# Kernel tuning notes

Hardware: AMD Instinct MI355X
Metric: run time of the kernel (lower is better)

Reference implementation:

```python
import jax, jax.numpy as jnp
import numpy as np

B, N, ATTR, H, OUT, STEPS = 8, 4096, 16, 64, 1, 8


def setup_inputs() -> dict:
    key = jax.random.key(0)
    ks = jax.random.split(key, 12)
    attr_matrix = jax.random.normal(ks[0], (B, N, ATTR), jnp.float32)
    adj_matrix = (jax.random.uniform(ks[1], (B, N, N)) < 0.01).astype(jnp.float32)
    s = float(1.0 / np.sqrt(H))
    u = lambda k, shape: jax.random.uniform(k, shape, jnp.float32, -s, s)
    Wi = jax.random.normal(ks[2], (H, ATTR), jnp.float32) * float(np.sqrt(2.0 / ATTR))  # kaiming
    bi = jnp.zeros((H,), jnp.float32)
    Wz = u(ks[3], (H, 3 * H)); bz = u(ks[4], (H,))
    Wr = u(ks[5], (H, 3 * H)); br = u(ks[6], (H,))
    Wh = u(ks[7], (H, 3 * H)); bh = u(ks[8], (H,))
    Wo = jax.random.normal(ks[9], (OUT, H), jnp.float32) * float(np.sqrt(2.0 / (H + OUT)))  # xavier
    bo = jnp.zeros((OUT,), jnp.float32)
    return dict(attr_matrix=attr_matrix, adj_matrix=adj_matrix, Wi=Wi, bi=bi,
                Wz=Wz, bz=bz, Wr=Wr, br=br, Wh=Wh, bh=bh, Wo=Wo, bo=bo)


def reference(attr_matrix, adj_matrix, Wi, bi, Wz, bz, Wr, br, Wh, bh, Wo, bo):
    # initial node states: (B, N, H)
    h = jax.nn.relu(attr_matrix @ Wi.T + bi)
    A_in = adj_matrix
    A_out = jnp.swapaxes(adj_matrix, -1, -2)
    for _ in range(STEPS):
        a_in = jnp.einsum('bij,bjh->bih', A_in, h)
        a_out = jnp.einsum('bij,bjh->bih', A_out, h)
        inp = jnp.concatenate([a_in, a_out], axis=-1)           # (B, N, 2H)
        xs = jnp.concatenate([inp, h], axis=-1)                  # (B, N, 3H)
        z = jax.nn.sigmoid(xs @ Wz.T + bz)
        r = jax.nn.sigmoid(xs @ Wr.T + br)
        hn = jnp.tanh(jnp.concatenate([inp, r * h], axis=-1) @ Wh.T + bh)
        h = (1.0 - z) * h + z * hn
    return h @ Wo.T + bo  # (B, N, OUT)
```

## Files before the change

kernel.cpp:

```cpp
#include <hip/hip_runtime.h>
#include <hip/hip_fp16.h>
#include <stdint.h>

#define BB 8
#define NN 4096
#define ATTRD 16
#define HD 64
#define STEPS 8
#define NODES (BB*NN)
#define ECAP 96
#define KPAD 196

typedef _Float16 half8 __attribute__((ext_vector_type(8)));
typedef float floatx4 __attribute__((ext_vector_type(4)));
typedef unsigned long long ull;

__global__ void init_h_kernel(const float* __restrict__ attr, const float* __restrict__ Wi,
                              const float* __restrict__ bi, float* __restrict__ h,
                              __half* __restrict__ h16) {
    int idx = blockIdx.x * blockDim.x + threadIdx.x;
    if (idx >= (NODES + 1) * HD) return;
    if (idx >= NODES * HD) {
        h16[idx] = __float2half(0.f);
        return;
    }
    int node = idx >> 6, l = idx & 63;
    const float* a = attr + node * ATTRD;
    const float* w = Wi + l * ATTRD;
    float acc = bi[l];
#pragma unroll
    for (int k = 0; k < ATTRD; k++) acc += a[k] * w[k];
    float r = acc > 0.f ? acc : 0.f;
    h[idx] = r;
    h16[idx] = __float2half(r);
}

__global__ void wprep_kernel(const float* __restrict__ Wz, const float* __restrict__ Wr,
                             const float* __restrict__ Wh,
                             _Float16* __restrict__ wf_hi, _Float16* __restrict__ wf_lo) {
    int t = blockIdx.x * blockDim.x + threadIdx.x;
    if (t >= 3 * 4 * 6 * 64 * 8) return;
    int mat = t / 12288, rem = t % 12288;
    int tile = rem / 3072, rem2 = rem % 3072;
    int kc = rem2 / 512, rem3 = rem2 % 512;
    int lane = rem3 / 8, j = rem3 % 8;
    int k = kc * 32 + (lane >> 4) * 8 + j;
    int och = tile * 16 + (lane & 15);
    const float* W = (mat == 0) ? Wz : (mat == 1) ? Wr : Wh;
    float v = W[och * 192 + k];
    _Float16 hi = (_Float16)v;
    wf_hi[t] = hi;
    wf_lo[t] = (_Float16)(v - (float)hi);
}

__global__ __launch_bounds__(256) void count_rows_kernel(const float4* __restrict__ A4,
                                                         int* __restrict__ cnt_in,
                                                         int* __restrict__ edge_in,
                                                         int* __restrict__ cnt_out,
                                                         int* __restrict__ edge_out) {
    int wave = threadIdx.x >> 6, l = threadIdx.x & 63;
    int row = blockIdx.x * 4 + wave;
    const float4* rp = A4 + (size_t)row * 1024;
    ull mask_lt = (l == 63) ? ~0ull >> 1 : ((1ull << (l + 1)) - 1) >> 1;
    float4 v[16];
#pragma unroll
    for (int t = 0; t < 16; t++) v[t] = rp[t * 64 + l];
    int colbase = (row >> 12) << 12;
    int run = 0;
    int* erow = edge_in + row * ECAP;
#pragma unroll
    for (int t = 0; t < 16; t++) {
        ull b0 = __ballot(v[t].x != 0.f);
        ull b1 = __ballot(v[t].y != 0.f);
        ull b2 = __ballot(v[t].z != 0.f);
        ull b3 = __ballot(v[t].w != 0.f);
        int pre = __popcll(b0 & mask_lt) + __popcll(b1 & mask_lt) +
                  __popcll(b2 & mask_lt) + __popcll(b3 & mask_lt);
        float vv[4] = {v[t].x, v[t].y, v[t].z, v[t].w};
        int jbase = (t * 64 + l) * 4;
        int inner = 0;
#pragma unroll
        for (int q = 0; q < 4; q++) {
            if (vv[q] != 0.f) {
                int col = colbase | (jbase + q);
                int slot = run + pre + inner;
                if (slot < ECAP) erow[slot] = col;
                inner++;
                int s2 = atomicAdd(&cnt_out[col], 1);
                if (s2 < ECAP) edge_out[col * ECAP + s2] = row;
            }
        }
        run += __popcll(b0) + __popcll(b1) + __popcll(b2) + __popcll(b3);
    }
    if (l == 0) cnt_in[row] = run;
}

__global__ __launch_bounds__(256) void aggregate_kernel(
        const uint4* __restrict__ h4, const float* __restrict__ h,
        const int* __restrict__ cnt_in, const int* __restrict__ edge_in,
        const int* __restrict__ cnt_out, const int* __restrict__ edge_out,
        float* __restrict__ xs) {
    int bid = blockIdx.x;
    int batch = bid & 7;
    int group = bid >> 3;
    int wave = threadIdx.x >> 6;
    int node = (batch << 12) + group * 4 + wave;
    int l = threadIdx.x & 63;
    int sub = l >> 3;
    int part = l & 7;
    int ni = cnt_in[node];  if (ni > ECAP) ni = ECAP;
    int no = cnt_out[node]; if (no > ECAP) no = ECAP;
    const int* ei = edge_in + node * ECAP;
    const int* eo = edge_out + node * ECAP;
    int ei0 = ei[l], ei1 = ei[64 + (l & 31)];
    int eo0 = eo[l], eo1 = eo[64 + (l & 31)];
    float ai0 = 0.f, ai1 = 0.f, ai2 = 0.f, ai3 = 0.f, ai4 = 0.f, ai5 = 0.f, ai6 = 0.f, ai7 = 0.f;
    float ao0 = 0.f, ao1 = 0.f, ao2 = 0.f, ao3 = 0.f, ao4 = 0.f, ao5 = 0.f, ao6 = 0.f, ao7 = 0.f;
    int nmax = ni > no ? ni : no;
    for (int s = 0; s < nmax; s += 8) {
        int il = s + sub;
        int gi = (il < 64) ? __shfl(ei0, il) : __shfl(ei1, il - 64);
        int go = (il < 64) ? __shfl(eo0, il) : __shfl(eo1, il - 64);
        gi = (il < ni) ? gi : NODES;
        go = (il < no) ? go : NODES;
        uint4 gA = h4[(gi << 3) | part];
        uint4 gB = h4[(go << 3) | part];
        float2 pA0 = __half22float2(*(__half2*)&gA.x);
        float2 pA1 = __half22float2(*(__half2*)&gA.y);
        float2 pA2 = __half22float2(*(__half2*)&gA.z);
        float2 pA3 = __half22float2(*(__half2*)&gA.w);
        ai0 += pA0.x; ai1 += pA0.y; ai2 += pA1.x; ai3 += pA1.y;
        ai4 += pA2.x; ai5 += pA2.y; ai6 += pA3.x; ai7 += pA3.y;
        float2 pB0 = __half22float2(*(__half2*)&gB.x);
        float2 pB1 = __half22float2(*(__half2*)&gB.y);
        float2 pB2 = __half22float2(*(__half2*)&gB.z);
        float2 pB3 = __half22float2(*(__half2*)&gB.w);
        ao0 += pB0.x; ao1 += pB0.y; ao2 += pB1.x; ao3 += pB1.y;
        ao4 += pB2.x; ao5 += pB2.y; ao6 += pB3.x; ao7 += pB3.y;
    }
#pragma unroll
    for (int off = 8; off < 64; off <<= 1) {
        ai0 += __shfl_xor(ai0, off); ai1 += __shfl_xor(ai1, off);
        ai2 += __shfl_xor(ai2, off); ai3 += __shfl_xor(ai3, off);
        ai4 += __shfl_xor(ai4, off); ai5 += __shfl_xor(ai5, off);
        ai6 += __shfl_xor(ai6, off); ai7 += __shfl_xor(ai7, off);
        ao0 += __shfl_xor(ao0, off); ao1 += __shfl_xor(ao1, off);
        ao2 += __shfl_xor(ao2, off); ao3 += __shfl_xor(ao3, off);
        ao4 += __shfl_xor(ao4, off); ao5 += __shfl_xor(ao5, off);
        ao6 += __shfl_xor(ao6, off); ao7 += __shfl_xor(ao7, off);
    }
    if (l < 8) {
        float* dst = xs + node * 192;
        float4 si0 = {ai0, ai1, ai2, ai3};
        float4 si1 = {ai4, ai5, ai6, ai7};
        float4 so0 = {ao0, ao1, ao2, ao3};
        float4 so1 = {ao4, ao5, ao6, ao7};
        *(float4*)(dst + l * 8)          = si0;
        *(float4*)(dst + l * 8 + 4)      = si1;
        *(float4*)(dst + 64 + l * 8)     = so0;
        *(float4*)(dst + 64 + l * 8 + 4) = so1;
    }
    xs[node * 192 + 128 + l] = h[(node << 6) | l];
}

__global__ __launch_bounds__(256) void gate_kernel(
        const float* __restrict__ xs_g,
        const _Float16* __restrict__ wf_hi, const _Float16* __restrict__ wf_lo,
        const float* __restrict__ bz, const float* __restrict__ br,
        const float* __restrict__ bh,
        float* __restrict__ h, __half* __restrict__ h16) {
    __shared__ float xs_t[16][KPAD];
    int bid = blockIdx.x;
    int base = ((bid & 7) << 12) | ((bid >> 3) << 4);
    int tid = threadIdx.x;
    {
        const float4* src = (const float4*)(xs_g + base * 192);
#pragma unroll
        for (int i = 0; i < 3; i++) {
            int idx = tid + i * 256;
            float4 v = src[idx];
            int nl = idx / 48, kb = (idx % 48) * 4;
            *(float4*)&xs_t[nl][kb] = v;
        }
    }
    __syncthreads();
    int wave = tid >> 6, lane = tid & 63;
    int m = lane & 15, q = lane >> 4;
    int ch = wave * 16 + m;
    const half8* WH = (const half8*)wf_hi;
    const half8* WL = (const half8*)wf_lo;

    floatx4 accz = {0.f, 0.f, 0.f, 0.f};
    floatx4 accr = {0.f, 0.f, 0.f, 0.f};
#pragma unroll
    for (int kc = 0; kc < 6; kc++) {
        const float* xr = &xs_t[m][kc * 32 + q * 8];
        float4 xa = *(const float4*)xr;
        float4 xb = *(const float4*)(xr + 4);
        float xv[8] = {xa.x, xa.y, xa.z, xa.w, xb.x, xb.y, xb.z, xb.w};
        half8 ahi, alo;
#pragma unroll
        for (int j = 0; j < 8; j++) {
            _Float16 hj = (_Float16)xv[j];
            ahi[j] = hj;
            alo[j] = (_Float16)(xv[j] - (float)hj);
        }
        half8 bzh = WH[((0 * 4 + wave) * 6 + kc) * 64 + lane];
        half8 bzl = WL[((0 * 4 + wave) * 6 + kc) * 64 + lane];
        half8 brh = WH[((1 * 4 + wave) * 6 + kc) * 64 + lane];
        half8 brl = WL[((1 * 4 + wave) * 6 + kc) * 64 + lane];
        accz = __builtin_amdgcn_mfma_f32_16x16x32_f16(ahi, bzh, accz, 0, 0, 0);
        accz = __builtin_amdgcn_mfma_f32_16x16x32_f16(alo, bzh, accz, 0, 0, 0);
        accz = __builtin_amdgcn_mfma_f32_16x16x32_f16(ahi, bzl, accz, 0, 0, 0);
        accr = __builtin_amdgcn_mfma_f32_16x16x32_f16(ahi, brh, accr, 0, 0, 0);
        accr = __builtin_amdgcn_mfma_f32_16x16x32_f16(alo, brh, accr, 0, 0, 0);
        accr = __builtin_amdgcn_mfma_f32_16x16x32_f16(ahi, brl, accr, 0, 0, 0);
    }
    float bzv = bz[ch], brv = br[ch], bhv = bh[ch];
    float zreg[4], hvreg[4], rh[4];
#pragma unroll
    for (int rg = 0; rg < 4; rg++) {
        int nl = q * 4 + rg;
        float z = 1.f / (1.f + __expf(-(accz[rg] + bzv)));
        float r = 1.f / (1.f + __expf(-(accr[rg] + brv)));
        float hv = xs_t[nl][128 + ch];
        zreg[rg] = z; hvreg[rg] = hv; rh[rg] = r * hv;
    }
    __syncthreads();
#pragma unroll
    for (int rg = 0; rg < 4; rg++) xs_t[q * 4 + rg][128 + ch] = rh[rg];
    __syncthreads();

    floatx4 acch = {0.f, 0.f, 0.f, 0.f};
#pragma unroll
    for (int kc = 0; kc < 6; kc++) {
        const float* xr = &xs_t[m][kc * 32 + q * 8];
        float4 xa = *(const float4*)xr;
        float4 xb = *(const float4*)(xr + 4);
        float xv[8] = {xa.x, xa.y, xa.z, xa.w, xb.x, xb.y, xb.z, xb.w};
        half8 ahi, alo;
#pragma unroll
        for (int j = 0; j < 8; j++) {
            _Float16 hj = (_Float16)xv[j];
            ahi[j] = hj;
            alo[j] = (_Float16)(xv[j] - (float)hj);
        }
        half8 bhh = WH[((2 * 4 + wave) * 6 + kc) * 64 + lane];
        half8 bhl = WL[((2 * 4 + wave) * 6 + kc) * 64 + lane];
        acch = __builtin_amdgcn_mfma_f32_16x16x32_f16(ahi, bhh, acch, 0, 0, 0);
        acch = __builtin_amdgcn_mfma_f32_16x16x32_f16(alo, bhh, acch, 0, 0, 0);
        acch = __builtin_amdgcn_mfma_f32_16x16x32_f16(ahi, bhl, acch, 0, 0, 0);
    }
    __syncthreads();
#pragma unroll
    for (int rg = 0; rg < 4; rg++) {
        int nl = q * 4 + rg;
        float pre = acch[rg] + bhv;
        float th = 2.f / (1.f + __expf(-2.f * pre)) - 1.f;
        float hv = hvreg[rg];
        xs_t[nl][ch] = hv + zreg[rg] * (th - hv);
    }
    __syncthreads();
    {
        int f = tid * 4;
        int nl = f >> 6, c = f & 63;
        float4 v = *(const float4*)&xs_t[nl][c];
        int gi = ((base + nl) << 6) | c;
        *(float4*)&h[gi] = v;
        __half2 p0 = {__float2half(v.x), __float2half(v.y)};
        __half2 p1 = {__float2half(v.z), __float2half(v.w)};
        *(__half2*)&h16[gi] = p0;
        *(__half2*)&h16[gi + 2] = p1;
    }
}

__global__ void out_kernel(const float* __restrict__ h, const float* __restrict__ Wo,
                           const float* __restrict__ bo, float* __restrict__ out) {
    int wid = (blockIdx.x * blockDim.x + threadIdx.x) >> 6;
    int l = threadIdx.x & 63;
    if (wid >= NODES) return;
    float p = h[(wid << 6) | l] * Wo[l];
#pragma unroll
    for (int off = 32; off > 0; off >>= 1) p += __shfl_down(p, off);
    if (l == 0) out[wid] = p + bo[0];
}

extern "C" void kernel_launch(void* const* d_in, const int* in_sizes, int n_in,
                              void* d_out, int out_size, void* d_ws, size_t ws_size,
                              hipStream_t stream) {
    const float* attr = (const float*)d_in[0];
    const float* adj  = (const float*)d_in[1];
    const float* Wi   = (const float*)d_in[2];
    const float* bi   = (const float*)d_in[3];
    const float* Wz   = (const float*)d_in[4];
    const float* bz   = (const float*)d_in[5];
    const float* Wr   = (const float*)d_in[6];
    const float* br   = (const float*)d_in[7];
    const float* Wh   = (const float*)d_in[8];
    const float* bh   = (const float*)d_in[9];
    const float* Wo   = (const float*)d_in[10];
    const float* bo   = (const float*)d_in[11];
    float* out = (float*)d_out;

    char* ws = (char*)d_ws;
    size_t off = 0;
    auto carve = [&](size_t bytes) { void* p = ws + off; off = (off + bytes + 255) & ~(size_t)255; return p; };
    float* h      = (float*)carve((size_t)NODES * HD * 4);
    __half* h16   = (__half*)carve((size_t)(NODES + 1) * HD * 2);
    float* xs     = (float*)carve((size_t)NODES * 192 * 4);
    _Float16* wf_hi = (_Float16*)carve(3 * 4 * 6 * 64 * 8 * 2);
    _Float16* wf_lo = (_Float16*)carve(3 * 4 * 6 * 64 * 8 * 2);
    int* cnt_in   = (int*)carve((size_t)NODES * 4);
    int* cnt_out  = (int*)carve((size_t)NODES * 4);
    int* edge_in  = (int*)carve((size_t)NODES * ECAP * 4);
    int* edge_out = (int*)carve((size_t)NODES * ECAP * 4);

    hipMemsetAsync(cnt_out, 0, (size_t)NODES * 4, stream);

    init_h_kernel<<<((NODES + 1) * HD + 255) / 256, 256, 0, stream>>>(attr, Wi, bi, h, h16);
    wprep_kernel<<<(3 * 4 * 6 * 64 * 8 + 255) / 256, 256, 0, stream>>>(Wz, Wr, Wh, wf_hi, wf_lo);
    count_rows_kernel<<<NODES / 4, 256, 0, stream>>>((const float4*)adj, cnt_in, edge_in,
                                                     cnt_out, edge_out);

    for (int step = 0; step < STEPS; ++step) {
        aggregate_kernel<<<NODES / 4, 256, 0, stream>>>(
            (const uint4*)h16, h, cnt_in, edge_in, cnt_out, edge_out, xs);
        gate_kernel<<<NODES / 16, 256, 0, stream>>>(xs, wf_hi, wf_lo, bz, br, bh, h, h16);
    }
    out_kernel<<<NODES * HD / 256, 256, 0, stream>>>(h, Wo, bo, out);
}
```

Before: 1.182 ms.

## Fuse neighbor aggregation into the GRU gate kernel with ping-pong half buffers

Merges the separate aggregate and gate kernels into a single per-step kernel. Each wave now gathers neighbor sums for four nodes straight into the shared-memory xs tile, so the 192-wide fp32 xs array no longer makes a round trip through global memory and one launch per step is removed. The fp16 hidden-state copy is double-buffered between steps, because other blocks still read neighbor states while this block writes its new ones. The gather loop also handles 16 neighbors per iteration, giving more loads in flight. In exchange there are four times fewer blocks in the gather phase and each wave processes its nodes one after another, which may reduce latency hiding for the irregular loads.

```diff
diff --git a/kernel.cpp b/kernel.cpp
--- a/kernel.cpp
+++ b/kernel.cpp
@@ -17,11 +17,12 @@
 
 __global__ void init_h_kernel(const float* __restrict__ attr, const float* __restrict__ Wi,
                               const float* __restrict__ bi, float* __restrict__ h,
-                              __half* __restrict__ h16) {
+                              __half* __restrict__ h16a, __half* __restrict__ h16b) {
     int idx = blockIdx.x * blockDim.x + threadIdx.x;
     if (idx >= (NODES + 1) * HD) return;
     if (idx >= NODES * HD) {
-        h16[idx] = __float2half(0.f);
+        h16a[idx] = __float2half(0.f);
+        h16b[idx] = __float2half(0.f);
         return;
     }
     int node = idx >> 6, l = idx & 63;
@@ -32,7 +33,7 @@
     for (int k = 0; k < ATTRD; k++) acc += a[k] * w[k];
     float r = acc > 0.f ? acc : 0.f;
     h[idx] = r;
-    h16[idx] = __float2half(r);
+    h16a[idx] = __float2half(r);
 }
 
 __global__ void wprep_kernel(const float* __restrict__ Wz, const float* __restrict__ Wr,
@@ -95,96 +96,103 @@
     if (l == 0) cnt_in[row] = run;
 }
 
-__global__ __launch_bounds__(256) void aggregate_kernel(
-        const uint4* __restrict__ h4, const float* __restrict__ h,
+__global__ __launch_bounds__(256) void step_kernel(
+        const uint4* __restrict__ h4,
         const int* __restrict__ cnt_in, const int* __restrict__ edge_in,
         const int* __restrict__ cnt_out, const int* __restrict__ edge_out,
-        float* __restrict__ xs) {
-    int bid = blockIdx.x;
-    int batch = bid & 7;
-    int group = bid >> 3;
-    int wave = threadIdx.x >> 6;
-    int node = (batch << 12) + group * 4 + wave;
-    int l = threadIdx.x & 63;
-    int sub = l >> 3;
-    int part = l & 7;
-    int ni = cnt_in[node];  if (ni > ECAP) ni = ECAP;
-    int no = cnt_out[node]; if (no > ECAP) no = ECAP;
-    const int* ei = edge_in + node * ECAP;
-    const int* eo = edge_out + node * ECAP;
-    int ei0 = ei[l], ei1 = ei[64 + (l & 31)];
-    int eo0 = eo[l], eo1 = eo[64 + (l & 31)];
-    float ai0 = 0.f, ai1 = 0.f, ai2 = 0.f, ai3 = 0.f, ai4 = 0.f, ai5 = 0.f, ai6 = 0.f, ai7 = 0.f;
-    float ao0 = 0.f, ao1 = 0.f, ao2 = 0.f, ao3 = 0.f, ao4 = 0.f, ao5 = 0.f, ao6 = 0.f, ao7 = 0.f;
-    int nmax = ni > no ? ni : no;
-    for (int s = 0; s < nmax; s += 8) {
-        int il = s + sub;
-        int gi = (il < 64) ? __shfl(ei0, il) : __shfl(ei1, il - 64);
-        int go = (il < 64) ? __shfl(eo0, il) : __shfl(eo1, il - 64);
-        gi = (il < ni) ? gi : NODES;
-        go = (il < no) ? go : NODES;
-        uint4 gA = h4[(gi << 3) | part];
-        uint4 gB = h4[(go << 3) | part];
-        float2 pA0 = __half22float2(*(__half2*)&gA.x);
-        float2 pA1 = __half22float2(*(__half2*)&gA.y);
-        float2 pA2 = __half22float2(*(__half2*)&gA.z);
-        float2 pA3 = __half22float2(*(__half2*)&gA.w);
-        ai0 += pA0.x; ai1 += pA0.y; ai2 += pA1.x; ai3 += pA1.y;
-        ai4 += pA2.x; ai5 += pA2.y; ai6 += pA3.x; ai7 += pA3.y;
-        float2 pB0 = __half22float2(*(__half2*)&gB.x);
-        float2 pB1 = __half22float2(*(__half2*)&gB.y);
-        float2 pB2 = __half22float2(*(__half2*)&gB.z);
-        float2 pB3 = __half22float2(*(__half2*)&gB.w);
-        ao0 += pB0.x; ao1 += pB0.y; ao2 += pB1.x; ao3 += pB1.y;
-        ao4 += pB2.x; ao5 += pB2.y; ao6 += pB3.x; ao7 += pB3.y;
-    }
-#pragma unroll
-    for (int off = 8; off < 64; off <<= 1) {
-        ai0 += __shfl_xor(ai0, off); ai1 += __shfl_xor(ai1, off);
-        ai2 += __shfl_xor(ai2, off); ai3 += __shfl_xor(ai3, off);
-        ai4 += __shfl_xor(ai4, off); ai5 += __shfl_xor(ai5, off);
-        ai6 += __shfl_xor(ai6, off); ai7 += __shfl_xor(ai7, off);
-        ao0 += __shfl_xor(ao0, off); ao1 += __shfl_xor(ao1, off);
-        ao2 += __shfl_xor(ao2, off); ao3 += __shfl_xor(ao3, off);
-        ao4 += __shfl_xor(ao4, off); ao5 += __shfl_xor(ao5, off);
-        ao6 += __shfl_xor(ao6, off); ao7 += __shfl_xor(ao7, off);
-    }
-    if (l < 8) {
-        float* dst = xs + node * 192;
-        float4 si0 = {ai0, ai1, ai2, ai3};
-        float4 si1 = {ai4, ai5, ai6, ai7};
-        float4 so0 = {ao0, ao1, ao2, ao3};
-        float4 so1 = {ao4, ao5, ao6, ao7};
-        *(float4*)(dst + l * 8)          = si0;
-        *(float4*)(dst + l * 8 + 4)      = si1;
-        *(float4*)(dst + 64 + l * 8)     = so0;
-        *(float4*)(dst + 64 + l * 8 + 4) = so1;
-    }
-    xs[node * 192 + 128 + l] = h[(node << 6) | l];
-}
-
-__global__ __launch_bounds__(256) void gate_kernel(
-        const float* __restrict__ xs_g,
         const _Float16* __restrict__ wf_hi, const _Float16* __restrict__ wf_lo,
         const float* __restrict__ bz, const float* __restrict__ br,
         const float* __restrict__ bh,
-        float* __restrict__ h, __half* __restrict__ h16) {
+        float* __restrict__ h,
+        __half* __restrict__ h16o) {
     __shared__ float xs_t[16][KPAD];
     int bid = blockIdx.x;
     int base = ((bid & 7) << 12) | ((bid >> 3) << 4);
     int tid = threadIdx.x;
+    int wave = tid >> 6, l = tid & 63;
+
     {
-        const float4* src = (const float4*)(xs_g + base * 192);
-#pragma unroll
-        for (int i = 0; i < 3; i++) {
-            int idx = tid + i * 256;
-            float4 v = src[idx];
-            int nl = idx / 48, kb = (idx % 48) * 4;
-            *(float4*)&xs_t[nl][kb] = v;
+        int sub = l >> 3;
+        int part = l & 7;
+        for (int nn = 0; nn < 4; nn++) {
+            int row = wave * 4 + nn;
+            int node = base + row;
+            int ni = cnt_in[node];  if (ni > ECAP) ni = ECAP;
+            int no = cnt_out[node]; if (no > ECAP) no = ECAP;
+            const int* ei = edge_in + node * ECAP;
+            const int* eo = edge_out + node * ECAP;
+            int ei0 = ei[l], ei1 = ei[64 + (l & 31)];
+            int eo0 = eo[l], eo1 = eo[64 + (l & 31)];
+            float hslot = h[(node << 6) | l];
+            float ai0 = 0.f, ai1 = 0.f, ai2 = 0.f, ai3 = 0.f, ai4 = 0.f, ai5 = 0.f, ai6 = 0.f, ai7 = 0.f;
+            float ao0 = 0.f, ao1 = 0.f, ao2 = 0.f, ao3 = 0.f, ao4 = 0.f, ao5 = 0.f, ao6 = 0.f, ao7 = 0.f;
+            int nmax = ni > no ? ni : no;
+            for (int s = 0; s < nmax; s += 16) {
+                int ila = s + sub, ilb = s + 8 + sub;
+                int gia = (ila < 64) ? __shfl(ei0, ila) : __shfl(ei1, ila - 64);
+                int gib = (ilb < 64) ? __shfl(ei0, ilb) : __shfl(ei1, ilb - 64);
+                int goa = (ila < 64) ? __shfl(eo0, ila) : __shfl(eo1, ila - 64);
+                int gob = (ilb < 64) ? __shfl(eo0, ilb) : __shfl(eo1, ilb - 64);
+                gia = (ila < ni) ? gia : NODES;
+                gib = (ilb < ni) ? gib : NODES;
+                goa = (ila < no) ? goa : NODES;
+                gob = (ilb < no) ? gob : NODES;
+                uint4 gA = h4[(gia << 3) | part];
+                uint4 gB = h4[(gib << 3) | part];
+                uint4 gC = h4[(goa << 3) | part];
+                uint4 gD = h4[(gob << 3) | part];
+                float2 pA0 = __half22float2(*(__half2*)&gA.x);
+                float2 pA1 = __half22float2(*(__half2*)&gA.y);
+                float2 pA2 = __half22float2(*(__half2*)&gA.z);
+                float2 pA3 = __half22float2(*(__half2*)&gA.w);
+                ai0 += pA0.x; ai1 += pA0.y; ai2 += pA1.x; ai3 += pA1.y;
+                ai4 += pA2.x; ai5 += pA2.y; ai6 += pA3.x; ai7 += pA3.y;
+                float2 pB0 = __half22float2(*(__half2*)&gB.x);
+                float2 pB1 = __half22float2(*(__half2*)&gB.y);
+                float2 pB2 = __half22float2(*(__half2*)&gB.z);
+                float2 pB3 = __half22float2(*(__half2*)&gB.w);
+                ai0 += pB0.x; ai1 += pB0.y; ai2 += pB1.x; ai3 += pB1.y;
+                ai4 += pB2.x; ai5 += pB2.y; ai6 += pB3.x; ai7 += pB3.y;
+                float2 pC0 = __half22float2(*(__half2*)&gC.x);
+                float2 pC1 = __half22float2(*(__half2*)&gC.y);
+                float2 pC2 = __half22float2(*(__half2*)&gC.z);
+                float2 pC3 = __half22float2(*(__half2*)&gC.w);
+                ao0 += pC0.x; ao1 += pC0.y; ao2 += pC1.x; ao3 += pC1.y;
+                ao4 += pC2.x; ao5 += pC2.y; ao6 += pC3.x; ao7 += pC3.y;
+                float2 pD0 = __half22float2(*(__half2*)&gD.x);
+                float2 pD1 = __half22float2(*(__half2*)&gD.y);
+                float2 pD2 = __half22float2(*(__half2*)&gD.z);
+                float2 pD3 = __half22float2(*(__half2*)&gD.w);
+                ao0 += pD0.x; ao1 += pD0.y; ao2 += pD1.x; ao3 += pD1.y;
+                ao4 += pD2.x; ao5 += pD2.y; ao6 += pD3.x; ao7 += pD3.y;
+            }
+#pragma unroll
+            for (int off = 8; off < 64; off <<= 1) {
+                ai0 += __shfl_xor(ai0, off); ai1 += __shfl_xor(ai1, off);
+                ai2 += __shfl_xor(ai2, off); ai3 += __shfl_xor(ai3, off);
+                ai4 += __shfl_xor(ai4, off); ai5 += __shfl_xor(ai5, off);
+                ai6 += __shfl_xor(ai6, off); ai7 += __shfl_xor(ai7, off);
+                ao0 += __shfl_xor(ao0, off); ao1 += __shfl_xor(ao1, off);
+                ao2 += __shfl_xor(ao2, off); ao3 += __shfl_xor(ao3, off);
+                ao4 += __shfl_xor(ao4, off); ao5 += __shfl_xor(ao5, off);
+                ao6 += __shfl_xor(ao6, off); ao7 += __shfl_xor(ao7, off);
+            }
+            if (l < 8) {
+                float4 si0 = {ai0, ai1, ai2, ai3};
+                float4 si1 = {ai4, ai5, ai6, ai7};
+                float4 so0 = {ao0, ao1, ao2, ao3};
+                float4 so1 = {ao4, ao5, ao6, ao7};
+                *(float4*)&xs_t[row][l * 8]          = si0;
+                *(float4*)&xs_t[row][l * 8 + 4]      = si1;
+                *(float4*)&xs_t[row][64 + l * 8]     = so0;
+                *(float4*)&xs_t[row][64 + l * 8 + 4] = so1;
+            }
+            xs_t[row][128 + l] = hslot;
         }
     }
     __syncthreads();
-    int wave = tid >> 6, lane = tid & 63;
+
+    int lane = l;
     int m = lane & 15, q = lane >> 4;
     int ch = wave * 16 + m;
     const half8* WH = (const half8*)wf_hi;
@@ -269,8 +277,8 @@
         *(float4*)&h[gi] = v;
         __half2 p0 = {__float2half(v.x), __float2half(v.y)};
         __half2 p1 = {__float2half(v.z), __float2half(v.w)};
-        *(__half2*)&h16[gi] = p0;
-        *(__half2*)&h16[gi + 2] = p1;
+        *(__half2*)&h16o[gi] = p0;
+        *(__half2*)&h16o[gi + 2] = p1;
     }
 }
 
@@ -306,8 +314,8 @@
     size_t off = 0;
     auto carve = [&](size_t bytes) { void* p = ws + off; off = (off + bytes + 255) & ~(size_t)255; return p; };
     float* h      = (float*)carve((size_t)NODES * HD * 4);
-    __half* h16   = (__half*)carve((size_t)(NODES + 1) * HD * 2);
-    float* xs     = (float*)carve((size_t)NODES * 192 * 4);
+    __half* h16a  = (__half*)carve((size_t)(NODES + 1) * HD * 2);
+    __half* h16b  = (__half*)carve((size_t)(NODES + 1) * HD * 2);
     _Float16* wf_hi = (_Float16*)carve(3 * 4 * 6 * 64 * 8 * 2);
     _Float16* wf_lo = (_Float16*)carve(3 * 4 * 6 * 64 * 8 * 2);
     int* cnt_in   = (int*)carve((size_t)NODES * 4);
@@ -317,15 +325,17 @@
 
     hipMemsetAsync(cnt_out, 0, (size_t)NODES * 4, stream);
 
-    init_h_kernel<<<((NODES + 1) * HD + 255) / 256, 256, 0, stream>>>(attr, Wi, bi, h, h16);
+    init_h_kernel<<<((NODES + 1) * HD + 255) / 256, 256, 0, stream>>>(attr, Wi, bi, h, h16a, h16b);
     wprep_kernel<<<(3 * 4 * 6 * 64 * 8 + 255) / 256, 256, 0, stream>>>(Wz, Wr, Wh, wf_hi, wf_lo);
     count_rows_kernel<<<NODES / 4, 256, 0, stream>>>((const float4*)adj, cnt_in, edge_in,
                                                      cnt_out, edge_out);
 
     for (int step = 0; step < STEPS; ++step) {
-        aggregate_kernel<<<NODES / 4, 256, 0, stream>>>(
-            (const uint4*)h16, h, cnt_in, edge_in, cnt_out, edge_out, xs);
-        gate_kernel<<<NODES / 16, 256, 0, stream>>>(xs, wf_hi, wf_lo, bz, br, bh, h, h16);
+        const __half* hin = (step & 1) ? h16b : h16a;
+        __half* hout      = (step & 1) ? h16a : h16b;
+        step_kernel<<<NODES / 16, 256, 0, stream>>>(
+            (const uint4*)hin, cnt_in, edge_in, cnt_out, edge_out,
+            wf_hi, wf_lo, bz, br, bh, h, hout);
     }
     out_kernel<<<NODES * HD / 256, 256, 0, stream>>>(h, Wo, bo, out);
 }
```

Measured after the change: 1.130 ms (median of 2 runs). -4.4%, faster.
